# Kernel tuning notes

Hardware: AMD Instinct MI355X
Metric: run time of the kernel (lower is better)

## Reference

```python
import jax, jax.numpy as jnp
import numpy as np

K_INTERACT = 8  # k nearest context nodes per target hyperedge


def setup_inputs() -> dict:
    key = jax.random.key(0)
    ks = jax.random.split(key, 7)
    B, C, H, W = 4, 256, 64, 64
    s = 1.0 / np.sqrt(C).astype(np.float32)
    return {
        "X_target": jax.random.normal(ks[0], (B, C, H, W), jnp.float32),
        "X_context1": jax.random.normal(ks[1], (B, C, H, W), jnp.float32),
        "X_context2": jax.random.normal(ks[2], (B, C, H, W), jnp.float32),
        # HypergraphConv params: node2edge Linear (W1,b1), edge2node Linear (W2,b2)
        "W1": jax.random.normal(ks[3], (C, C), jnp.float32) * s,
        "b1": jax.random.normal(ks[4], (C,), jnp.float32) * s,
        "W2": jax.random.normal(ks[5], (C, C), jnp.float32) * s,
        "b2": jax.random.normal(ks[6], (C,), jnp.float32) * s,
    }


def _hypergraph_one(Xt, Xc, W1, b1, W2, b2, k):
    """Per-batch hypergraph message passing, sparse form of H^T X / H X.
    Xt: [N, C] target nodes, Xc: [Nc, C] context nodes.
    Edge j = {target j} U {k nearest context nodes of target j}.
    Equivalent to dense H_i [N+Nc, N] with degree normalization.
    """
    N, C = Xt.shape
    Nc = Xc.shape[0]
    # squared Euclidean cdist (same argmins as torch.cdist), knn = smallest-k
    d2 = (jnp.sum(Xt * Xt, axis=1)[:, None]
          + jnp.sum(Xc * Xc, axis=1)[None, :]
          - 2.0 * (Xt @ Xc.T))                      # [N, Nc]
    _, knn = jax.lax.top_k(-d2, k)                   # [N, k] context indices

    # node2edge linear transform on all nodes
    Xn_t = Xt @ W1 + b1                              # [N, C]
    Xn_c = Xc @ W1 + b1                              # [Nc, C]

    # X_edge = (H^T @ Xn) / deg_e ; deg_e = k+1 (self + k distinct knn)
    gathered = Xn_c[knn]                             # [N, k, C]
    X_edge = (Xn_t + gathered.sum(axis=1)) / jnp.float32(k + 1)

    # edge2node linear transform
    X_et = X_edge @ W2 + b2                          # [N, C]

    # X_node_new = (H @ X_et) / deg_v
    # target node v belongs only to edge v -> deg_v = 1
    out_t = X_et
    # context node c sums X_et[j] over edges j that selected it
    flat = knn.reshape(-1)                           # [N*k]
    contrib = jax.ops.segment_sum(
        jnp.broadcast_to(X_et[:, None, :], (N, k, C)).reshape(N * k, C),
        flat, num_segments=Nc)                       # [Nc, C]
    counts = jax.ops.segment_sum(jnp.ones((N * k,), jnp.float32),
                                 flat, num_segments=Nc)
    out_c = contrib / jnp.clip(counts, 1.0)[:, None]  # deg_v clamp_min(1)
    return out_t, out_c


def reference(X_target, X_context1, X_context2, W1, b1, W2, b2):
    B, C, H, W = X_target.shape
    N = H * W
    to_nodes = lambda x: x.transpose(0, 2, 3, 1).reshape(B, N, C)
    Xt = to_nodes(X_target)                                       # [B, N, C]
    Xc = jnp.concatenate([to_nodes(X_context1), to_nodes(X_context2)],
                         axis=1)                                  # [B, 2N, C]
    f = lambda xt, xc: _hypergraph_one(xt, xc, W1, b1, W2, b2, K_INTERACT)
    out_t, out_c = jax.vmap(f)(Xt, Xc)
    to_img = lambda x: x.reshape(B, H, W, C).transpose(0, 3, 1, 2)
    return (to_img(out_t), to_img(out_c[:, :N]), to_img(out_c[:, N:]))
```

## Files before the change

kernel.cpp:

```cpp
#include <hip/hip_runtime.h>
#include <math.h>
#include <float.h>

#define BATCH 4
#define CH    256
#define NT    4096
#define NCTX  8192
#define KI    8

#define CSEL    10
#define DNSPLIT 8
#define CTX_PER (NCTX / DNSPLIT)
#define NTILE   (CTX_PER / 32)
#define NKEY    (DNSPLIT * CSEL)
#define RESC    12

typedef __attribute__((ext_vector_type(8)))  __bf16 bf16x8;
typedef __attribute__((ext_vector_type(16))) float  f32x16;

__device__ __forceinline__ unsigned short bf16_rne(float v) {
  unsigned u = __float_as_uint(v);
  return (unsigned short)((u + 0x7fffu + ((u >> 16) & 1u)) >> 16);
}

__global__ __launch_bounds__(256) void k_prep(const float* __restrict__ Xt,
                                              const float* __restrict__ Xc1,
                                              const float* __restrict__ Xc2,
                                              float* __restrict__ Q,
                                              float* __restrict__ P,
                                              unsigned short* __restrict__ XtBh,
                                              unsigned short* __restrict__ XtBl,
                                              unsigned short* __restrict__ XcBh,
                                              unsigned short* __restrict__ XcBl,
                                              float* __restrict__ nrm,
                                              const float* __restrict__ W1,
                                              const float* __restrict__ W2,
                                              unsigned short* __restrict__ WT1h,
                                              unsigned short* __restrict__ WT1l,
                                              unsigned short* __restrict__ WT2h,
                                              unsigned short* __restrict__ WT2l) {
  __shared__ float tile[128][33];
  __shared__ float ps[8][32];
  const int bid = blockIdx.x;
  const int tx = threadIdx.x, ty = threadIdx.y;

  if (bid < 3072) {
    const int x = bid & 127, y = (bid >> 7) & 1, z = bid >> 8;
    const int which = z >> 2, b = z & 3;
    const float* src;
    float* dF; unsigned short *dH, *dL; float* nrmp = nullptr;
    if (which == 0) {
      src = Xt + (long)b * CH * NT;
      dF = Q + (long)b * NT * CH;
      dH = XtBh + (long)b * NT * CH;  dL = XtBl + (long)b * NT * CH;
    } else if (which == 1) {
      src = Xc1 + (long)b * CH * NT;
      dF = P + (long)b * NCTX * CH;
      dH = XcBh + (long)b * NCTX * CH;  dL = XcBl + (long)b * NCTX * CH;
      nrmp = nrm + (long)b * NCTX;
    } else {
      src = Xc2 + (long)b * CH * NT;
      dF = P + ((long)b * NCTX + NT) * CH;
      dH = XcBh + ((long)b * NCTX + NT) * CH;  dL = XcBl + ((long)b * NCTX + NT) * CH;
      nrmp = nrm + (long)b * NCTX + NT;
    }
    const int m0 = x * 32, c0 = y * 128;
    float part = 0.f;
#pragma unroll
    for (int i = ty; i < 128; i += 8) {
      float v = src[(long)(c0 + i) * NT + (m0 + tx)];
      tile[i][tx] = v;
      part = fmaf(v, v, part);
    }
    if (which) ps[ty][tx] = part;
    __syncthreads();
#pragma unroll
    for (int i = ty; i < 32; i += 8) {
      float v0 = tile[4 * tx + 0][i];
      float v1 = tile[4 * tx + 1][i];
      float v2 = tile[4 * tx + 2][i];
      float v3 = tile[4 * tx + 3][i];
      long o = (long)(m0 + i) * CH + (c0 + 4 * tx);
      float4 f4; f4.x = v0; f4.y = v1; f4.z = v2; f4.w = v3;
      *(float4*)&dF[o] = f4;
      unsigned short h0 = bf16_rne(v0), h1 = bf16_rne(v1), h2 = bf16_rne(v2), h3 = bf16_rne(v3);
      ushort4 h4; h4.x = h0; h4.y = h1; h4.z = h2; h4.w = h3;
      *(ushort4*)&dH[o] = h4;
      ushort4 l4;
      l4.x = bf16_rne(v0 - __uint_as_float((unsigned)h0 << 16));
      l4.y = bf16_rne(v1 - __uint_as_float((unsigned)h1 << 16));
      l4.z = bf16_rne(v2 - __uint_as_float((unsigned)h2 << 16));
      l4.w = bf16_rne(v3 - __uint_as_float((unsigned)h3 << 16));
      *(ushort4*)&dL[o] = l4;
    }
    if (which && ty == 0) {
      float s = 0.f;
#pragma unroll
      for (int j = 0; j < 8; ++j) s += ps[j][tx];
      atomicAdd(&nrmp[m0 + tx], -0.5f * s);
    }
  } else {
    const int r = bid - 3072;
    const int n0 = (r & 7) * 32, k0 = ((r >> 3) & 7) * 32;
    const float* W = (r >> 6) ? W2 : W1;
    unsigned short* WTh = (r >> 6) ? WT2h : WT1h;
    unsigned short* WTl = (r >> 6) ? WT2l : WT1l;
#pragma unroll
    for (int i = ty; i < 32; i += 8)
      tile[i][tx] = W[(k0 + i) * CH + (n0 + tx)];
    __syncthreads();
#pragma unroll
    for (int i = ty; i < 32; i += 8) {
      float v = tile[tx][i];
      int o = (n0 + i) * CH + (k0 + tx);
      unsigned short h = bf16_rne(v);
      WTh[o] = h;
      WTl[o] = bf16_rne(v - __uint_as_float((unsigned)h << 16));
    }
  }
}

__global__ __launch_bounds__(256) void k_main(const __bf16* __restrict__ XcB,
                                              const __bf16* __restrict__ XtB,
                                              const float* __restrict__ nrm,
                                              unsigned* __restrict__ cand,
                                              const unsigned short* __restrict__ XtBh,
                                              const unsigned short* __restrict__ XtBl,
                                              const unsigned short* __restrict__ XcBh,
                                              const unsigned short* __restrict__ XcBl,
                                              const unsigned short* __restrict__ WTh,
                                              const unsigned short* __restrict__ WTl,
                                              const float* __restrict__ bias,
                                              float* __restrict__ outT,
                                              float* __restrict__ outC) {
  __shared__ __bf16 lds[2][32 * CH];
  const int bid = blockIdx.x;
  const int t = threadIdx.x, w = t >> 6, lane = t & 63;
  const int l31 = lane & 31, lh = lane >> 5;

  if (bid < 1024) {
    const int xk = bid & 7;
    const int b = xk >> 1, jh = xk & 1;
    const int jw = (bid >> 3) & 15, split = bid >> 7;
    const int tgt0 = (jh * 16 + jw) * 128 + w * 32;
    const int cbase = split * CTX_PER;
    const float* nrmt = nrm + (long)b * NCTX + cbase;

    const __bf16* tp = XtB + ((long)b * NT + tgt0 + l31) * CH + lh * 8;
    bf16x8 bfrag[16];
#pragma unroll
    for (int s = 0; s < 16; ++s) bfrag[s] = *(const bf16x8*)(tp + s * 16);

    unsigned kd[CSEL];
#pragma unroll
    for (int q = 0; q < CSEL; ++q) kd[q] = 0xFFFFFFFFu;

    const __bf16* cp = XcB + ((long)b * NCTX + cbase + l31) * CH;

    auto STAGE = [&](int buf, int jt) {
#pragma unroll
      for (int r = 0; r < 4; ++r) {
        int c = r * 4 + w;
        const __bf16* src = cp + (long)jt * 32 * CH + (c * 2 + lh) * 8;
        __bf16* dst = &lds[buf][c * 512];
        __builtin_amdgcn_global_load_lds((const __attribute__((address_space(1))) void*)src,
                                         (__attribute__((address_space(3))) void*)dst,
                                         16, 0, 0);
      }
    };

    STAGE(0, 0);
    __syncthreads();

    int cur = 0;
    for (int jt = 0; jt < NTILE; ++jt) {
      if (jt + 1 < NTILE) STAGE(cur ^ 1, jt + 1);

      const int ct0 = jt * 32;
      f32x16 acc;
#pragma unroll
      for (int g = 0; g < 4; ++g) {
        float4 nv = *(const float4*)&nrmt[ct0 + 8 * g + 4 * lh];
        acc[4 * g + 0] = nv.x; acc[4 * g + 1] = nv.y;
        acc[4 * g + 2] = nv.z; acc[4 * g + 3] = nv.w;
      }
#pragma unroll
      for (int s = 0; s < 16; ++s) {
        bf16x8 a = *(const bf16x8*)(&lds[cur][s * 512 + lane * 8]);
        acc = __builtin_amdgcn_mfma_f32_32x32x16_bf16(a, bfrag[s], acc, 0, 0, 0);
      }

#pragma unroll
      for (int reg = 0; reg < 16; ++reg) {
        const int row = (reg & 3) + 8 * (reg >> 2) + lh * 4;
        float sc = fmaf(acc[reg], -2.0f, 512.0f);
        unsigned key = (__float_as_uint(sc) & 0xFFFFF800u) | (unsigned)ct0 | (unsigned)row;
#pragma unroll
        for (int q = 0; q < CSEL; ++q) {
          unsigned lo = min(key, kd[q]);
          key = max(key, kd[q]);
          kd[q] = lo;
        }
      }
      __syncthreads();
      cur ^= 1;
    }

    unsigned oth[CSEL];
#pragma unroll
    for (int q = 0; q < CSEL; ++q) oth[q] = (unsigned)__shfl_xor((int)kd[q], 32, 64);
    if (lh == 0) {
      long ob = (((long)b * NT + tgt0 + l31) * DNSPLIT + split) * CSEL;
#pragma unroll
      for (int q = 0; q < CSEL; ++q)
        cand[ob + q] = min(kd[q], oth[CSEL - 1 - q]);
    }
  } else {
    int g = bid - 1024;
    const unsigned short *Ah, *Al; float* out; int M, m0, b;
    if (g < 512) { Ah = XtBh; Al = XtBl; out = outT; M = NT;   m0 = (g & 127) * 32; b = g >> 7; }
    else { g -= 512; Ah = XcBh; Al = XcBl; out = outC; M = NCTX; m0 = (g & 255) * 32; b = g >> 8; }
    __bf16* ldsH = lds[0];
    __bf16* ldsL = lds[1];
    const long abase = (long)b * M * CH;
    const unsigned short* pH = Ah + abase + (long)(m0 + l31) * CH;
    const unsigned short* pL = Al + abase + (long)(m0 + l31) * CH;
#pragma unroll
    for (int r = 0; r < 4; ++r) {
      int c = r * 4 + w;
      __builtin_amdgcn_global_load_lds(
          (const __attribute__((address_space(1))) void*)(pH + (c * 2 + lh) * 8),
          (__attribute__((address_space(3))) void*)&ldsH[c * 512], 16, 0, 0);
      __builtin_amdgcn_global_load_lds(
          (const __attribute__((address_space(1))) void*)(pL + (c * 2 + lh) * 8),
          (__attribute__((address_space(3))) void*)&ldsL[c * 512], 16, 0, 0);
    }
    __syncthreads();

    const int n0 = w * 64;
    f32x16 acc0, acc1;
#pragma unroll
    for (int i = 0; i < 16; ++i) { acc0[i] = 0.f; acc1[i] = 0.f; }
#pragma unroll
    for (int s = 0; s < 16; ++s) {
      bf16x8 ah = *(const bf16x8*)&ldsH[s * 512 + lane * 8];
      bf16x8 al = *(const bf16x8*)&ldsL[s * 512 + lane * 8];
      const int koff = lh * 8 + s * 16;
      bf16x8 bh0 = *(const bf16x8*)&WTh[(n0 + l31) * CH + koff];
      bf16x8 bl0 = *(const bf16x8*)&WTl[(n0 + l31) * CH + koff];
      bf16x8 bh1 = *(const bf16x8*)&WTh[(n0 + 32 + l31) * CH + koff];
      bf16x8 bl1 = *(const bf16x8*)&WTl[(n0 + 32 + l31) * CH + koff];
      acc0 = __builtin_amdgcn_mfma_f32_32x32x16_bf16(ah, bh0, acc0, 0, 0, 0);
      acc1 = __builtin_amdgcn_mfma_f32_32x32x16_bf16(ah, bh1, acc1, 0, 0, 0);
      acc0 = __builtin_amdgcn_mfma_f32_32x32x16_bf16(ah, bl0, acc0, 0, 0, 0);
      acc1 = __builtin_amdgcn_mfma_f32_32x32x16_bf16(ah, bl1, acc1, 0, 0, 0);
      acc0 = __builtin_amdgcn_mfma_f32_32x32x16_bf16(al, bh0, acc0, 0, 0, 0);
      acc1 = __builtin_amdgcn_mfma_f32_32x32x16_bf16(al, bh1, acc1, 0, 0, 0);
    }
    float* ob = out + abase;
    float bi0 = bias[n0 + l31], bi1 = bias[n0 + 32 + l31];
#pragma unroll
    for (int reg = 0; reg < 16; ++reg) {
      int row = (reg & 3) + 8 * (reg >> 2) + 4 * lh;
      ob[(long)(m0 + row) * CH + n0 + l31]      = acc0[reg] + bi0;
      ob[(long)(m0 + row) * CH + n0 + 32 + l31] = acc1[reg] + bi1;
    }
  }
}

__global__ __launch_bounds__(256) void k_gemm_mfma(const unsigned short* __restrict__ Ah,
                                                   const unsigned short* __restrict__ Al,
                                                   const unsigned short* __restrict__ WTh,
                                                   const unsigned short* __restrict__ WTl,
                                                   const float* __restrict__ bias,
                                                   float* __restrict__ out, int M) {
  __shared__ __bf16 ldsH[32 * CH];
  __shared__ __bf16 ldsL[32 * CH];
  const int b = blockIdx.y;
  const int m0 = blockIdx.x * 32;
  const int t = threadIdx.x, w = t >> 6, lane = t & 63;
  const int l31 = lane & 31, lh = lane >> 5;
  const long abase = (long)b * M * CH;
  const unsigned short* pH = Ah + abase + (long)(m0 + l31) * CH;
  const unsigned short* pL = Al + abase + (long)(m0 + l31) * CH;
#pragma unroll
  for (int r = 0; r < 4; ++r) {
    int c = r * 4 + w;
    __builtin_amdgcn_global_load_lds(
        (const __attribute__((address_space(1))) void*)(pH + (c * 2 + lh) * 8),
        (__attribute__((address_space(3))) void*)&ldsH[c * 512], 16, 0, 0);
    __builtin_amdgcn_global_load_lds(
        (const __attribute__((address_space(1))) void*)(pL + (c * 2 + lh) * 8),
        (__attribute__((address_space(3))) void*)&ldsL[c * 512], 16, 0, 0);
  }
  __syncthreads();

  const int n0 = w * 64;
  f32x16 acc0, acc1;
#pragma unroll
  for (int i = 0; i < 16; ++i) { acc0[i] = 0.f; acc1[i] = 0.f; }
#pragma unroll
  for (int s = 0; s < 16; ++s) {
    bf16x8 ah = *(const bf16x8*)&ldsH[s * 512 + lane * 8];
    bf16x8 al = *(const bf16x8*)&ldsL[s * 512 + lane * 8];
    const int koff = lh * 8 + s * 16;
    bf16x8 bh0 = *(const bf16x8*)&WTh[(n0 + l31) * CH + koff];
    bf16x8 bl0 = *(const bf16x8*)&WTl[(n0 + l31) * CH + koff];
    bf16x8 bh1 = *(const bf16x8*)&WTh[(n0 + 32 + l31) * CH + koff];
    bf16x8 bl1 = *(const bf16x8*)&WTl[(n0 + 32 + l31) * CH + koff];
    acc0 = __builtin_amdgcn_mfma_f32_32x32x16_bf16(ah, bh0, acc0, 0, 0, 0);
    acc1 = __builtin_amdgcn_mfma_f32_32x32x16_bf16(ah, bh1, acc1, 0, 0, 0);
    acc0 = __builtin_amdgcn_mfma_f32_32x32x16_bf16(ah, bl0, acc0, 0, 0, 0);
    acc1 = __builtin_amdgcn_mfma_f32_32x32x16_bf16(ah, bl1, acc1, 0, 0, 0);
    acc0 = __builtin_amdgcn_mfma_f32_32x32x16_bf16(al, bh0, acc0, 0, 0, 0);
    acc1 = __builtin_amdgcn_mfma_f32_32x32x16_bf16(al, bh1, acc1, 0, 0, 0);
  }
  float* ob = out + abase;
  float bi0 = bias[n0 + l31], bi1 = bias[n0 + 32 + l31];
#pragma unroll
  for (int reg = 0; reg < 16; ++reg) {
    int row = (reg & 3) + 8 * (reg >> 2) + 4 * lh;
    ob[(long)(m0 + row) * CH + n0 + l31]      = acc0[reg] + bi0;
    ob[(long)(m0 + row) * CH + n0 + 32 + l31] = acc1[reg] + bi1;
  }
}

__global__ __launch_bounds__(64) void k_rescore(const float* __restrict__ XtT,
                                                const float* __restrict__ XcT,
                                                const unsigned* __restrict__ cand,
                                                int* __restrict__ knn,
                                                unsigned* __restrict__ counts) {
  const int n = blockIdx.x, b = blockIdx.y, lane = threadIdx.x;
  const int grp = lane >> 4, gl = lane & 15;
  __shared__ unsigned sk[NKEY];
  __shared__ int cidx[RESC];
  __shared__ double sd[RESC];
  __shared__ int sj[RESC];
  const unsigned* kp = cand + ((long)b * NT + n) * NKEY;
  unsigned k0 = kp[lane];
  unsigned k1 = (lane < NKEY - 64) ? kp[64 + lane] : 0xFFFFFFFFu;
  sk[lane] = k0;
  if (lane < NKEY - 64) sk[64 + lane] = k1;
  __syncthreads();
  int r0 = 0, r1 = 0;
  for (int i = 0; i < NKEY; ++i) {
    unsigned s = sk[i];
    r0 += (s < k0 || (s == k0 && i < lane)) ? 1 : 0;
    r1 += (s < k1 || (s == k1 && i < 64 + lane)) ? 1 : 0;
  }
  if (r0 < RESC) cidx[r0] = (lane / CSEL) * CTX_PER + (int)(k0 & 0x7FFu);
  if (lane < NKEY - 64 && r1 < RESC)
    cidx[r1] = ((64 + lane) / CSEL) * CTX_PER + (int)(k1 & 0x7FFu);
  __syncthreads();

  const float* xt = XtT + ((long)b * NT + n) * CH + gl * 16;
  double xa[16];
#pragma unroll
  for (int r = 0; r < 4; ++r) {
    float4 v = *(const float4*)(xt + r * 4);
    xa[4 * r + 0] = (double)v.x; xa[4 * r + 1] = (double)v.y;
    xa[4 * r + 2] = (double)v.z; xa[4 * r + 3] = (double)v.w;
  }
#pragma unroll
  for (int q0 = 0; q0 < RESC; q0 += 4) {
    int q = q0 + grp;
    int j = cidx[q];
    const float* xc = XcT + ((long)b * NCTX + j) * CH + gl * 16;
    double acc = 0.0;
#pragma unroll
    for (int r = 0; r < 4; ++r) {
      float4 v = *(const float4*)(xc + r * 4);
      double d0 = xa[4 * r + 0] - (double)v.x; acc = fma(d0, d0, acc);
      double d1 = xa[4 * r + 1] - (double)v.y; acc = fma(d1, d1, acc);
      double d2 = xa[4 * r + 2] - (double)v.z; acc = fma(d2, d2, acc);
      double d3 = xa[4 * r + 3] - (double)v.w; acc = fma(d3, d3, acc);
    }
#pragma unroll
    for (int off = 8; off > 0; off >>= 1) acc += __shfl_xor(acc, off, 64);
    if (gl == 0) { sd[q] = acc; sj[q] = j; }
  }
  __syncthreads();
  double dq = (lane < RESC) ? sd[lane] : DBL_MAX;
  int    jq = (lane < RESC) ? sj[lane] : 0x7fffffff;
  int rank = 0;
#pragma unroll
  for (int i = 0; i < RESC; ++i) {
    double di = sd[i]; int ji = sj[i];
    rank += (di < dq || (di == dq && ji < jq)) ? 1 : 0;
  }
  if (lane < RESC && rank < KI) {
    knn[((long)b * NT + n) * KI + rank] = jq;
    atomicAdd(&counts[(long)b * NCTX + jq], 1u);
  }
}

__global__ __launch_bounds__(256) void k_gather(const float* __restrict__ Xn_t,
                                                const float* __restrict__ Xn_c,
                                                const int* __restrict__ knn,
                                                unsigned short* __restrict__ XeH,
                                                unsigned short* __restrict__ XeL) {
  const int n = blockIdx.x, b = blockIdx.y, c = threadIdx.x;
  const int* kn = knn + ((long)b * NT + n) * KI;
  int j[KI];
#pragma unroll
  for (int q = 0; q < KI; ++q) j[q] = kn[q];
  float acc = Xn_t[((long)b * NT + n) * CH + c];
#pragma unroll
  for (int q = 0; q < KI; ++q) acc += Xn_c[((long)b * NCTX + j[q]) * CH + c];
  float xe = acc / 9.0f;
  long o = ((long)b * NT + n) * CH + c;
  unsigned short h = bf16_rne(xe);
  XeH[o] = h;
  XeL[o] = bf16_rne(xe - __uint_as_float((unsigned)h << 16));
}

__global__ __launch_bounds__(256) void k_g2f(const unsigned short* __restrict__ XeH_g,
                                             const unsigned short* __restrict__ XeL_g,
                                             const unsigned short* __restrict__ WTh,
                                             const unsigned short* __restrict__ WTl,
                                             const float* __restrict__ bias,
                                             float* __restrict__ out_t,
                                             float* __restrict__ R) {
  __shared__ char smem[34816];
  __bf16* ldsH = (__bf16*)smem;
  __bf16* ldsL = (__bf16*)(smem + 16384);
  const int b = blockIdx.y;
  const int m0 = blockIdx.x * 32;
  const int t = threadIdx.x, w = t >> 6, lane = t & 63;
  const int l31 = lane & 31, lh = lane >> 5;
  const long abase = (long)b * NT * CH;
  const unsigned short* pH = XeH_g + abase + (long)(m0 + l31) * CH;
  const unsigned short* pL = XeL_g + abase + (long)(m0 + l31) * CH;
#pragma unroll
  for (int r = 0; r < 4; ++r) {
    int c = r * 4 + w;
    __builtin_amdgcn_global_load_lds(
        (const __attribute__((address_space(1))) void*)(pH + (c * 2 + lh) * 8),
        (__attribute__((address_space(3))) void*)&ldsH[c * 512], 16, 0, 0);
    __builtin_amdgcn_global_load_lds(
        (const __attribute__((address_space(1))) void*)(pL + (c * 2 + lh) * 8),
        (__attribute__((address_space(3))) void*)&ldsL[c * 512], 16, 0, 0);
  }
  __syncthreads();

  const unsigned short* wh0 = WTh + (long)(w * 64 + l31) * CH;
  const unsigned short* wl0 = WTl + (long)(w * 64 + l31) * CH;
  f32x16 acc0, acc1;
#pragma unroll
  for (int i = 0; i < 16; ++i) { acc0[i] = 0.f; acc1[i] = 0.f; }
#pragma unroll
  for (int s = 0; s < 16; ++s) {
    const int koff = lh * 8 + s * 16;
    bf16x8 beh = *(const bf16x8*)&ldsH[s * 512 + lane * 8];
    bf16x8 bel = *(const bf16x8*)&ldsL[s * 512 + lane * 8];
    bf16x8 ah0 = *(const bf16x8*)(const __bf16*)(wh0 + koff);
    bf16x8 al0 = *(const bf16x8*)(const __bf16*)(wl0 + koff);
    bf16x8 ah1 = *(const bf16x8*)(const __bf16*)(wh0 + 32 * CH + koff);
    bf16x8 al1 = *(const bf16x8*)(const __bf16*)(wl0 + 32 * CH + koff);
    acc0 = __builtin_amdgcn_mfma_f32_32x32x16_bf16(ah0, beh, acc0, 0, 0, 0);
    acc1 = __builtin_amdgcn_mfma_f32_32x32x16_bf16(ah1, beh, acc1, 0, 0, 0);
    acc0 = __builtin_amdgcn_mfma_f32_32x32x16_bf16(al0, beh, acc0, 0, 0, 0);
    acc1 = __builtin_amdgcn_mfma_f32_32x32x16_bf16(al1, beh, acc1, 0, 0, 0);
    acc0 = __builtin_amdgcn_mfma_f32_32x32x16_bf16(ah0, bel, acc0, 0, 0, 0);
    acc1 = __builtin_amdgcn_mfma_f32_32x32x16_bf16(ah1, bel, acc1, 0, 0, 0);
  }
  __syncthreads();

  float* S = (float*)smem;
  float* ot = out_t + (long)b * CH * NT + m0;
#pragma unroll
  for (int reg = 0; reg < 16; ++reg) {
    const int row = (reg & 3) + 8 * (reg >> 2) + 4 * lh;
    const int ch0 = w * 64 + row, ch1 = ch0 + 32;
    float v0 = acc0[reg] + bias[ch0];
    float v1 = acc1[reg] + bias[ch1];
    S[ch0 * 33 + l31] = v0;
    S[ch1 * 33 + l31] = v1;
    ot[(long)ch0 * NT + l31] = v0;
    ot[(long)ch1 * NT + l31] = v1;
  }
  __syncthreads();
  const int n = t & 31, cg = t >> 5;
  float* rrow = R + ((long)b * NT + m0 + n) * CH;
#pragma unroll
  for (int kk = 0; kk < 8; ++kk) {
    const int c = cg * 32 + kk * 4;
    float4 v;
    v.x = S[(c + 0) * 33 + n];
    v.y = S[(c + 1) * 33 + n];
    v.z = S[(c + 2) * 33 + n];
    v.w = S[(c + 3) * 33 + n];
    *(float4*)(rrow + c) = v;
  }
}

__global__ __launch_bounds__(256) void k_scatter(const float* __restrict__ Xet,
                                                 const int* __restrict__ knn,
                                                 float* __restrict__ contrib) {
  const int n = blockIdx.x, b = blockIdx.y, c = threadIdx.x;
  const float v = Xet[((long)b * NT + n) * CH + c];
  const int* kn = knn + ((long)b * NT + n) * KI;
#pragma unroll
  for (int q = 0; q < KI; ++q)
    atomicAdd(&contrib[((long)b * NCTX + kn[q]) * CH + c], v);
}

__global__ __launch_bounds__(256) void k_fin_c(const float* __restrict__ contrib,
                                               const unsigned* __restrict__ counts,
                                               float* __restrict__ out1,
                                               float* __restrict__ out2) {
  __shared__ float tile[128][33];
  const int b = blockIdx.z;
  const int j0 = blockIdx.x * 128, c0 = blockIdx.y * 32;
  const int tx = threadIdx.x, ty = threadIdx.y;
#pragma unroll
  for (int i = ty; i < 128; i += 8) {
    float cnt = fmaxf((float)counts[(long)b * NCTX + j0 + i], 1.0f);
    tile[i][tx] = contrib[((long)b * NCTX + j0 + i) * CH + c0 + tx] * (1.0f / cnt);
  }
  __syncthreads();
  float* outp = (j0 < NT) ? (out1 + (long)b * CH * NT + j0)
                          : (out2 + (long)b * CH * NT + (j0 - NT));
#pragma unroll
  for (int i = ty; i < 32; i += 8) {
    float4 v;
    v.x = tile[4 * tx + 0][i];
    v.y = tile[4 * tx + 1][i];
    v.z = tile[4 * tx + 2][i];
    v.w = tile[4 * tx + 3][i];
    *(float4*)&outp[(long)(c0 + i) * NT + 4 * tx] = v;
  }
}

extern "C" void kernel_launch(void* const* d_in, const int* in_sizes, int n_in,
                              void* d_out, int out_size, void* d_ws, size_t ws_size,
                              hipStream_t stream) {
  const float* Xt  = (const float*)d_in[0];
  const float* Xc1 = (const float*)d_in[1];
  const float* Xc2 = (const float*)d_in[2];
  const float* W1  = (const float*)d_in[3];
  const float* b1  = (const float*)d_in[4];
  const float* W2  = (const float*)d_in[5];
  const float* b2  = (const float*)d_in[6];
  float* out = (float*)d_out;

  float* P = (float*)d_ws;
  float* Q = P + (long)BATCH * NCTX * CH;
  float* R = Q + (long)BATCH * NT * CH;
  float* nrm = R + (long)BATCH * NT * CH;
  unsigned* counts = (unsigned*)(nrm + (long)BATCH * NCTX);
  int* knn = (int*)(counts + (long)BATCH * NCTX);
  unsigned short* WT1h = (unsigned short*)(knn + (long)BATCH * NT * KI);
  unsigned short* WT1l = WT1h + CH * CH;
  unsigned short* WT2h = WT1l + CH * CH;
  unsigned short* WT2l = WT2h + CH * CH;
  float* Xn_c_fat = (float*)(WT2l + CH * CH);
  unsigned* cand_fat = (unsigned*)(Xn_c_fat + (long)BATCH * NCTX * CH);
  const size_t need_fat = (size_t)((char*)(cand_fat + (long)BATCH * NT * NKEY) - (char*)d_ws);
  const bool fat = ws_size >= need_fat;

  unsigned* cand = fat ? cand_fat : (unsigned*)R;
  float* Xn_c = fat ? Xn_c_fat : P;
  float* Xn_t = R;

  unsigned short* XcBh = (unsigned short*)d_out;
  unsigned short* XtBh = XcBh + (long)BATCH * NCTX * CH;
  unsigned short* XcBl = XtBh + (long)BATCH * NT * CH;
  unsigned short* XtBl = XcBl + (long)BATCH * NCTX * CH;

  unsigned short* XeH = (unsigned short*)Q;
  unsigned short* XeL = XeH + (long)BATCH * NT * CH;

  float* out_t  = out;
  float* out_c1 = out + (long)BATCH * CH * NT;
  float* out_c2 = out + 2L * BATCH * CH * NT;

  dim3 tb(32, 8);

  hipMemsetAsync(nrm, 0, (size_t)BATCH * NCTX * 8, stream);

  k_prep<<<dim3(3072 + 128), tb, 0, stream>>>(Xt, Xc1, Xc2, Q, P, XtBh, XtBl, XcBh, XcBl, nrm,
                                              W1, W2, WT1h, WT1l, WT2h, WT2l);

  if (fat) {
    k_main<<<dim3(1024 + 512 + 1024), 256, 0, stream>>>(
        (const __bf16*)XcBh, (const __bf16*)XtBh, nrm, cand,
        XtBh, XtBl, XcBh, XcBl, WT1h, WT1l, b1, Xn_t, Xn_c);
    k_rescore<<<dim3(NT, BATCH), 64, 0, stream>>>(Q, P, cand, knn, counts);
  } else {
    k_main<<<dim3(1024), 256, 0, stream>>>(
        (const __bf16*)XcBh, (const __bf16*)XtBh, nrm, cand,
        XtBh, XtBl, XcBh, XcBl, WT1h, WT1l, b1, Xn_t, Xn_c);
    k_rescore<<<dim3(NT, BATCH), 64, 0, stream>>>(Q, P, cand, knn, counts);
    k_gemm_mfma<<<dim3(NT / 32, BATCH), 256, 0, stream>>>(XtBh, XtBl, WT1h, WT1l, b1, Xn_t, NT);
    k_gemm_mfma<<<dim3(NCTX / 32, BATCH), 256, 0, stream>>>(XcBh, XcBl, WT1h, WT1l, b1, Xn_c, NCTX);
  }

  k_gather<<<dim3(NT, BATCH), 256, 0, stream>>>(Xn_t, Xn_c, knn, XeH, XeL);

  hipMemsetAsync(P, 0, (size_t)BATCH * NCTX * CH * 4, stream);

  k_g2f<<<dim3(NT / 32, BATCH), 256, 0, stream>>>(XeH, XeL, WT2h, WT2l, b2, out_t, R);

  k_scatter<<<dim3(NT, BATCH), 256, 0, stream>>>(R, knn, P);
  k_fin_c<<<dim3(NCTX / 128, CH / 32, BATCH), tb, 0, stream>>>(P, counts, out_c1, out_c2);
}
```

Before: 399.8 us.

## Fuse scatter into edge2node GEMM, interleave fat k_main blocks, batch rescore

```diff
diff --git a/kernel.cpp b/kernel.cpp
--- a/kernel.cpp
+++ b/kernel.cpp
@@ -132,16 +132,24 @@
                                               const unsigned short* __restrict__ WTl,
                                               const float* __restrict__ bias,
                                               float* __restrict__ outT,
-                                              float* __restrict__ outC) {
+                                              float* __restrict__ outC,
+                                              int fatmode) {
   __shared__ __bf16 lds[2][32 * CH];
   const int bid = blockIdx.x;
   const int t = threadIdx.x, w = t >> 6, lane = t & 63;
   const int l31 = lane & 31, lh = lane >> 5;
 
-  if (bid < 1024) {
-    const int xk = bid & 7;
+  int lid = bid, gid = -1;
+  if (fatmode) {
+    const int group = bid / 5, slot = bid % 5;
+    if (slot < 2) lid = group * 2 + slot;
+    else { lid = -1; gid = group * 3 + (slot - 2); }
+  }
+
+  if (gid < 0) {
+    const int xk = lid & 7;
     const int b = xk >> 1, jh = xk & 1;
-    const int jw = (bid >> 3) & 15, split = bid >> 7;
+    const int jw = (lid >> 3) & 15, split = lid >> 7;
     const int tgt0 = (jh * 16 + jw) * 128 + w * 32;
     const int cbase = split * CTX_PER;
     const float* nrmt = nrm + (long)b * NCTX + cbase;
@@ -216,7 +224,7 @@
         cand[ob + q] = min(kd[q], oth[CSEL - 1 - q]);
     }
   } else {
-    int g = bid - 1024;
+    int g = gid;
     const unsigned short *Ah, *Al; float* out; int M, m0, b;
     if (g < 512) { Ah = XtBh; Al = XtBl; out = outT; M = NT;   m0 = (g & 127) * 32; b = g >> 7; }
     else { g -= 512; Ah = XcBh; Al = XcBl; out = outC; M = NCTX; m0 = (g & 255) * 32; b = g >> 8; }
@@ -325,32 +333,33 @@
   }
 }
 
-__global__ __launch_bounds__(64) void k_rescore(const float* __restrict__ XtT,
-                                                const float* __restrict__ XcT,
-                                                const unsigned* __restrict__ cand,
-                                                int* __restrict__ knn,
-                                                unsigned* __restrict__ counts) {
-  const int n = blockIdx.x, b = blockIdx.y, lane = threadIdx.x;
+__global__ __launch_bounds__(256) void k_rescore(const float* __restrict__ XtT,
+                                                 const float* __restrict__ XcT,
+                                                 const unsigned* __restrict__ cand,
+                                                 int* __restrict__ knn,
+                                                 unsigned* __restrict__ counts) {
+  const int t = threadIdx.x, sub = t >> 6, lane = t & 63;
+  const int n = blockIdx.x * 4 + sub, b = blockIdx.y;
   const int grp = lane >> 4, gl = lane & 15;
-  __shared__ unsigned sk[NKEY];
-  __shared__ int cidx[RESC];
-  __shared__ double sd[RESC];
-  __shared__ int sj[RESC];
+  __shared__ unsigned sk[4][NKEY];
+  __shared__ int cidx[4][RESC];
+  __shared__ double sd[4][RESC];
+  __shared__ int sj[4][RESC];
   const unsigned* kp = cand + ((long)b * NT + n) * NKEY;
   unsigned k0 = kp[lane];
   unsigned k1 = (lane < NKEY - 64) ? kp[64 + lane] : 0xFFFFFFFFu;
-  sk[lane] = k0;
-  if (lane < NKEY - 64) sk[64 + lane] = k1;
+  sk[sub][lane] = k0;
+  if (lane < NKEY - 64) sk[sub][64 + lane] = k1;
   __syncthreads();
   int r0 = 0, r1 = 0;
   for (int i = 0; i < NKEY; ++i) {
-    unsigned s = sk[i];
+    unsigned s = sk[sub][i];
     r0 += (s < k0 || (s == k0 && i < lane)) ? 1 : 0;
     r1 += (s < k1 || (s == k1 && i < 64 + lane)) ? 1 : 0;
   }
-  if (r0 < RESC) cidx[r0] = (lane / CSEL) * CTX_PER + (int)(k0 & 0x7FFu);
+  if (r0 < RESC) cidx[sub][r0] = (lane / CSEL) * CTX_PER + (int)(k0 & 0x7FFu);
   if (lane < NKEY - 64 && r1 < RESC)
-    cidx[r1] = ((64 + lane) / CSEL) * CTX_PER + (int)(k1 & 0x7FFu);
+    cidx[sub][r1] = ((64 + lane) / CSEL) * CTX_PER + (int)(k1 & 0x7FFu);
   __syncthreads();
 
   const float* xt = XtT + ((long)b * NT + n) * CH + gl * 16;
@@ -364,7 +373,7 @@
 #pragma unroll
   for (int q0 = 0; q0 < RESC; q0 += 4) {
     int q = q0 + grp;
-    int j = cidx[q];
+    int j = cidx[sub][q];
     const float* xc = XcT + ((long)b * NCTX + j) * CH + gl * 16;
     double acc = 0.0;
 #pragma unroll
@@ -377,15 +386,15 @@
     }
 #pragma unroll
     for (int off = 8; off > 0; off >>= 1) acc += __shfl_xor(acc, off, 64);
-    if (gl == 0) { sd[q] = acc; sj[q] = j; }
-  }
-  __syncthreads();
-  double dq = (lane < RESC) ? sd[lane] : DBL_MAX;
-  int    jq = (lane < RESC) ? sj[lane] : 0x7fffffff;
+    if (gl == 0) { sd[sub][q] = acc; sj[sub][q] = j; }
+  }
+  __syncthreads();
+  double dq = (lane < RESC) ? sd[sub][lane] : DBL_MAX;
+  int    jq = (lane < RESC) ? sj[sub][lane] : 0x7fffffff;
   int rank = 0;
 #pragma unroll
   for (int i = 0; i < RESC; ++i) {
-    double di = sd[i]; int ji = sj[i];
+    double di = sd[sub][i]; int ji = sj[sub][i];
     rank += (di < dq || (di == dq && ji < jq)) ? 1 : 0;
   }
   if (lane < RESC && rank < KI) {
@@ -419,9 +428,11 @@
                                              const unsigned short* __restrict__ WTh,
                                              const unsigned short* __restrict__ WTl,
                                              const float* __restrict__ bias,
+                                             const int* __restrict__ knn,
                                              float* __restrict__ out_t,
-                                             float* __restrict__ R) {
+                                             float* __restrict__ contrib) {
   __shared__ char smem[34816];
+  __shared__ int knns[256];
   __bf16* ldsH = (__bf16*)smem;
   __bf16* ldsL = (__bf16*)(smem + 16384);
   const int b = blockIdx.y;
@@ -441,6 +452,7 @@
         (const __attribute__((address_space(1))) void*)(pL + (c * 2 + lh) * 8),
         (__attribute__((address_space(3))) void*)&ldsL[c * 512], 16, 0, 0);
   }
+  knns[t] = knn[((long)b * NT + m0 + (t >> 3)) * KI + (t & 7)];
   __syncthreads();
 
   const unsigned short* wh0 = WTh + (long)(w * 64 + l31) * CH;
@@ -480,29 +492,16 @@
     ot[(long)ch1 * NT + l31] = v1;
   }
   __syncthreads();
-  const int n = t & 31, cg = t >> 5;
-  float* rrow = R + ((long)b * NT + m0 + n) * CH;
-#pragma unroll
-  for (int kk = 0; kk < 8; ++kk) {
-    const int c = cg * 32 + kk * 4;
-    float4 v;
-    v.x = S[(c + 0) * 33 + n];
-    v.y = S[(c + 1) * 33 + n];
-    v.z = S[(c + 2) * 33 + n];
-    v.w = S[(c + 3) * 33 + n];
-    *(float4*)(rrow + c) = v;
-  }
-}
-
-__global__ __launch_bounds__(256) void k_scatter(const float* __restrict__ Xet,
-                                                 const int* __restrict__ knn,
-                                                 float* __restrict__ contrib) {
-  const int n = blockIdx.x, b = blockIdx.y, c = threadIdx.x;
-  const float v = Xet[((long)b * NT + n) * CH + c];
-  const int* kn = knn + ((long)b * NT + n) * KI;
-#pragma unroll
-  for (int q = 0; q < KI; ++q)
-    atomicAdd(&contrib[((long)b * NCTX + kn[q]) * CH + c], v);
+
+  float* cb = contrib + (long)b * NCTX * CH;
+#pragma unroll 4
+  for (int nn = 0; nn < 32; ++nn) {
+    float v = S[t * 33 + nn];
+    const int* kn = &knns[nn * 8];
+#pragma unroll
+    for (int q = 0; q < KI; ++q)
+      atomicAdd(&cb[(long)kn[q] * CH + t], v);
+  }
 }
 
 __global__ __launch_bounds__(256) void k_fin_c(const float* __restrict__ contrib,
@@ -583,15 +582,15 @@
                                               W1, W2, WT1h, WT1l, WT2h, WT2l);
 
   if (fat) {
-    k_main<<<dim3(1024 + 512 + 1024), 256, 0, stream>>>(
+    k_main<<<dim3(2560), 256, 0, stream>>>(
         (const __bf16*)XcBh, (const __bf16*)XtBh, nrm, cand,
-        XtBh, XtBl, XcBh, XcBl, WT1h, WT1l, b1, Xn_t, Xn_c);
-    k_rescore<<<dim3(NT, BATCH), 64, 0, stream>>>(Q, P, cand, knn, counts);
+        XtBh, XtBl, XcBh, XcBl, WT1h, WT1l, b1, Xn_t, Xn_c, 1);
+    k_rescore<<<dim3(NT / 4, BATCH), 256, 0, stream>>>(Q, P, cand, knn, counts);
   } else {
     k_main<<<dim3(1024), 256, 0, stream>>>(
         (const __bf16*)XcBh, (const __bf16*)XtBh, nrm, cand,
-        XtBh, XtBl, XcBh, XcBl, WT1h, WT1l, b1, Xn_t, Xn_c);
-    k_rescore<<<dim3(NT, BATCH), 64, 0, stream>>>(Q, P, cand, knn, counts);
+        XtBh, XtBl, XcBh, XcBl, WT1h, WT1l, b1, Xn_t, Xn_c, 0);
+    k_rescore<<<dim3(NT / 4, BATCH), 256, 0, stream>>>(Q, P, cand, knn, counts);
     k_gemm_mfma<<<dim3(NT / 32, BATCH), 256, 0, stream>>>(XtBh, XtBl, WT1h, WT1l, b1, Xn_t, NT);
     k_gemm_mfma<<<dim3(NCTX / 32, BATCH), 256, 0, stream>>>(XcBh, XcBl, WT1h, WT1l, b1, Xn_c, NCTX);
   }
@@ -600,8 +599,7 @@
 
   hipMemsetAsync(P, 0, (size_t)BATCH * NCTX * CH * 4, stream);
 
-  k_g2f<<<dim3(NT / 32, BATCH), 256, 0, stream>>>(XeH, XeL, WT2h, WT2l, b2, out_t, R);
-
-  k_scatter<<<dim3(NT, BATCH), 256, 0, stream>>>(R, knn, P);
+  k_g2f<<<dim3(NT / 32, BATCH), 256, 0, stream>>>(XeH, XeL, WT2h, WT2l, b2, knn, out_t, P);
+
   k_fin_c<<<dim3(NCTX / 128, CH / 32, BATCH), tb, 0, stream>>>(P, counts, out_c1, out_c2);
 }
```

Result: slower. 439.3 us (+9.9%).
